# Kernel tuning notes

Measured on AMD Instinct MI355X. Metric: run time of the kernel, lower is better.

The kernel has to match this reference:

```python
import jax, jax.numpy as jnp
import numpy as np

HID = 64

def _rnn_layer(x, W_ih, W_hh, b_ih, b_hh):
    # x: [B, T, F]; PyTorch RNN step: h_t = tanh(x_t @ W_ih.T + b_ih + h_{t-1} @ W_hh.T + b_hh)
    # Precompute the input projection for all timesteps as one big GEMM.
    x_proj = jnp.einsum('btf,hf->bth', x, W_ih) + b_ih  # [B, T, H]
    B = x.shape[0]
    h0 = jnp.zeros((B, HID), x.dtype)

    def step(h, xt):
        h = jnp.tanh(xt + h @ W_hh.T + b_hh)
        return h, h

    _, hs = jax.lax.scan(step, h0, jnp.swapaxes(x_proj, 0, 1))  # hs: [T, B, H]
    return jnp.swapaxes(hs, 0, 1)  # [B, T, H]


def setup_inputs() -> dict:
    key = jax.random.key(0)
    ks = jax.random.split(key, 20)
    B, T, F = 4096, 128, 14
    s_in = 1.0 / np.sqrt(HID)  # PyTorch RNN init scale
    d = {
        'x': jax.random.normal(ks[0], (B, T, F), jnp.float32),
        'W_ih0': jax.random.normal(ks[1], (HID, F), jnp.float32) * s_in,
        'W_hh0': jax.random.normal(ks[2], (HID, HID), jnp.float32) * s_in,
        'b_ih0': jax.random.normal(ks[3], (HID,), jnp.float32) * s_in,
        'b_hh0': jax.random.normal(ks[4], (HID,), jnp.float32) * s_in,
        'W_ih1': jax.random.normal(ks[5], (HID, HID), jnp.float32) * s_in,
        'W_hh1': jax.random.normal(ks[6], (HID, HID), jnp.float32) * s_in,
        'b_ih1': jax.random.normal(ks[7], (HID,), jnp.float32) * s_in,
        'b_hh1': jax.random.normal(ks[8], (HID,), jnp.float32) * s_in,
        'W_ih2': jax.random.normal(ks[9], (HID, HID), jnp.float32) * s_in,
        'W_hh2': jax.random.normal(ks[10], (HID, HID), jnp.float32) * s_in,
        'b_ih2': jax.random.normal(ks[11], (HID,), jnp.float32) * s_in,
        'b_hh2': jax.random.normal(ks[12], (HID,), jnp.float32) * s_in,
        'fc1_w': jax.random.normal(ks[13], (32, HID), jnp.float32) * s_in,
        'fc1_b': jax.random.normal(ks[14], (32,), jnp.float32) * s_in,
        'fc2_w': jax.random.normal(ks[15], (1, 32), jnp.float32) * (1.0 / np.sqrt(32)),
        'fc2_b': jax.random.normal(ks[16], (1,), jnp.float32) * (1.0 / np.sqrt(32)),
    }
    return d


def reference(x, W_ih0, W_hh0, b_ih0, b_hh0, W_ih1, W_hh1, b_ih1, b_hh1,
              W_ih2, W_hh2, b_ih2, b_hh2, fc1_w, fc1_b, fc2_w, fc2_b):
    h = _rnn_layer(x, W_ih0, W_hh0, b_ih0, b_hh0)
    h = _rnn_layer(h, W_ih1, W_hh1, b_ih1, b_hh1)
    h = _rnn_layer(h, W_ih2, W_hh2, b_ih2, b_hh2)
    last = h[:, -1, :]                       # [B, H]
    y = jax.nn.relu(last @ fc1_w.T + fc1_b)  # [B, 32]
    return y @ fc2_w.T + fc2_b               # [B, 1]
```

## Files before the change

kernel.cpp:

```cpp
#include <hip/hip_runtime.h>

typedef short  s16x8 __attribute__((ext_vector_type(8)));
typedef float  f32x4 __attribute__((ext_vector_type(4)));
typedef float  f32x2 __attribute__((ext_vector_type(2)));
typedef unsigned int u32;
typedef unsigned int u32x4 __attribute__((ext_vector_type(4)));
typedef unsigned short u16;

#define DEVI static __device__ __forceinline__

#if __has_builtin(__builtin_amdgcn_exp2f)
#define EXP2(v) __builtin_amdgcn_exp2f(v)
#else
#define EXP2(v) exp2f(v)
#endif

constexpr int T_  = 128;
constexpr int F_  = 14;
constexpr int H_  = 64;
constexpr int BPB = 16;
constexpr int K_  = 8;
constexpr int NCH = T_ / K_;

constexpr int HF_BYTES   = 2 * 2 * K_ * 2 * 64 * 16;
constexpr int XBUF_BYTES = 2 * K_ * 64 * 16;
constexpr int SMEM_BYTES = HF_BYTES + XBUF_BYTES;

DEVI u16 f2bf(float f) {
  u32 u = __builtin_bit_cast(u32, f);
  u += 0x7fffu + ((u >> 16) & 1u);
  return (u16)(u >> 16);
}
DEVI u32 cvtpk(float a, float b) {
  u32 r;
  asm("v_cvt_pk_bf16_f32 %0, %1, %2" : "=v"(r) : "v"(a), "v"(b));
  return r;
}
DEVI s16x8 packfrag(const f32x4& a, const f32x4& b) {
  u32x4 p;
  p[0] = cvtpk(a[0], a[1]); p[1] = cvtpk(a[2], a[3]);
  p[2] = cvtpk(b[0], b[1]); p[3] = cvtpk(b[2], b[3]);
  return __builtin_bit_cast(s16x8, p);
}
DEVI f32x4 tanh4(const f32x4& v) {
  const f32x4 kC = -2.8853900817779268f;
  f32x4 t = v * kC;
  f32x4 e;
  e[0] = EXP2(t[0]); e[1] = EXP2(t[1]);
  e[2] = EXP2(t[2]); e[3] = EXP2(t[3]);
  const f32x4 kOne = 1.0f;
  f32x4 d = e + kOne;
  f32x4 r;
  r[0] = __builtin_amdgcn_rcpf(d[0]); r[1] = __builtin_amdgcn_rcpf(d[1]);
  r[2] = __builtin_amdgcn_rcpf(d[2]); r[3] = __builtin_amdgcn_rcpf(d[3]);
  const f32x4 kTwo = 2.0f, kNegOne = -1.0f;
  return __builtin_elementwise_fma(kTwo, r, kNegOne);
}
DEVI f32x4 MFMA(s16x8 a, s16x8 b, f32x4 c) {
  return __builtin_amdgcn_mfma_f32_16x16x32_bf16(a, b, c, 0, 0, 0);
}
DEVI s16x8 ldrow8(const float* p) {
  const f32x4 a = ((const f32x4*)p)[0];
  const f32x4 b = ((const f32x4*)p)[1];
  s16x8 r;
  r[0] = (short)f2bf(a[0]); r[1] = (short)f2bf(a[1]);
  r[2] = (short)f2bf(a[2]); r[3] = (short)f2bf(a[3]);
  r[4] = (short)f2bf(b[0]); r[5] = (short)f2bf(b[1]);
  r[6] = (short)f2bf(b[2]); r[7] = (short)f2bf(b[3]);
  return r;
}

__global__ __launch_bounds__(256, 1) void rnn_ck(
    const float* __restrict__ x,
    const float* __restrict__ Wih0, const float* __restrict__ Whh0,
    const float* __restrict__ bih0, const float* __restrict__ bhh0,
    const float* __restrict__ Wih1, const float* __restrict__ Whh1,
    const float* __restrict__ bih1, const float* __restrict__ bhh1,
    const float* __restrict__ Wih2, const float* __restrict__ Whh2,
    const float* __restrict__ bih2, const float* __restrict__ bhh2,
    const float* __restrict__ fc1w, const float* __restrict__ fc1b,
    const float* __restrict__ fc2w, const float* __restrict__ fc2b,
    float* __restrict__ out)
{
  extern __shared__ __align__(16) char smem[];
  u32x4 (*hf)[2][K_][2][64] = (u32x4 (*)[2][K_][2][64])smem;
  u32x4 (*xbuf)[K_][64]     = (u32x4 (*)[K_][64])(smem + HF_BYTES);

  const int tid  = threadIdx.x;
  const int w    = tid >> 6;
  const int lane = tid & 63;
  const int g    = lane >> 4;
  const int m    = lane & 15;
  const int b0   = blockIdx.x * BPB;

  f32x4 z4; z4[0] = 0.f; z4[1] = 0.f; z4[2] = 0.f; z4[3] = 0.f;

  s16x8 Ax[4], Ai[4][2], Ah[4][2];
  f32x4 bc[4];
  if (w < 3) {
    const float* Wi = Wih1; const float* Wh = Whh0;
    const float* bi = bih0; const float* bh = bhh0;
    if (w == 1)      { Wi = Wih1; Wh = Whh1; bi = bih1; bh = bhh1; }
    else if (w == 2) { Wi = Wih2; Wh = Whh2; bi = bih2; bh = bhh2; }
    #pragma unroll
    for (int n = 0; n < 4; n++) {
      const int Lr = 32 * (n & 1) + 8 * (m >> 2) + 4 * (n >> 1) + (m & 3);
      if (w == 0) {
        s16x8 r;
        #pragma unroll
        for (int j2 = 0; j2 < 8; j2++) {
          const int kk = 8 * g + j2;
          r[j2] = (kk < F_) ? (short)f2bf(Wih0[Lr * F_ + kk]) : (short)0;
        }
        Ax[n] = r;
        Ai[n][0] = r; Ai[n][1] = r;
      } else {
        #pragma unroll
        for (int kt = 0; kt < 2; kt++)
          Ai[n][kt] = ldrow8(Wi + Lr * H_ + 32 * kt + 8 * g);
        Ax[n] = Ai[n][0];
      }
      #pragma unroll
      for (int kt = 0; kt < 2; kt++)
        Ah[n][kt] = ldrow8(Wh + Lr * H_ + 32 * kt + 8 * g);
      const int Lb = 32 * (n & 1) + 8 * g + 4 * (n >> 1);
      bc[n] = *(const f32x4*)(bi + Lb) + *(const f32x4*)(bh + Lb);
    }
  }

  s16x8 F[2];
  {
    s16x8 z;
    #pragma unroll
    for (int i = 0; i < 8; i++) z[i] = 0;
    F[0] = z; F[1] = z;
  }
  f32x4 h2v[4];
  #pragma unroll
  for (int n = 0; n < 4; n++) h2v[n] = z4;

  const float* xrow = x + (size_t)(b0 + m) * T_ * F_;
  auto ldraw = [&](int t, f32x4& ra, f32x4& rb) {
    const float* p = xrow + t * F_;
    if (g == 0) {
      f32x2 p0 = *(const f32x2*)(p),     p1 = *(const f32x2*)(p + 2);
      f32x2 p2 = *(const f32x2*)(p + 4), p3 = *(const f32x2*)(p + 6);
      ra[0] = p0[0]; ra[1] = p0[1]; ra[2] = p1[0]; ra[3] = p1[1];
      rb[0] = p2[0]; rb[1] = p2[1]; rb[2] = p3[0]; rb[3] = p3[1];
    } else if (g == 1) {
      f32x2 p4 = *(const f32x2*)(p + 8), p5 = *(const f32x2*)(p + 10);
      f32x2 p6 = *(const f32x2*)(p + 12);
      ra[0] = p4[0]; ra[1] = p4[1]; ra[2] = p5[0]; ra[3] = p5[1];
      rb[0] = p6[0]; rb[1] = p6[1]; rb[2] = 0.f;   rb[3] = 0.f;
    } else {
      ra = z4; rb = z4;
    }
  };
  auto cvtraw = [&](const f32x4& ra, const f32x4& rb) -> s16x8 {
    u32x4 p;
    p[0] = cvtpk(ra[0], ra[1]); p[1] = cvtpk(ra[2], ra[3]);
    p[2] = cvtpk(rb[0], rb[1]); p[3] = cvtpk(rb[2], rb[3]);
    return __builtin_bit_cast(s16x8, p);
  };

  if (w == 3) {
    f32x4 ra[K_], rb[K_];
    #pragma unroll
    for (int k = 0; k < K_; k++) ldraw(k, ra[k], rb[k]);
    #pragma unroll
    for (int k = 0; k < K_; k++)
      xbuf[0][k][lane] = __builtin_bit_cast(u32x4, cvtraw(ra[k], rb[k]));
  }
  __syncthreads();

  #pragma unroll 1
  for (int e = 0; e < NCH + 2; e++) {
    const int wb = e & 1, rbuf = wb ^ 1;

    if (w == 3) {
      if (e < NCH - 1) {
        f32x4 ra[K_], rb[K_];
        #pragma unroll
        for (int k = 0; k < K_; k++) ldraw((e + 1) * K_ + k, ra[k], rb[k]);
        #pragma unroll
        for (int k = 0; k < K_; k++)
          xbuf[rbuf][k][lane] = __builtin_bit_cast(u32x4, cvtraw(ra[k], rb[k]));
      }
    } else {
      const int c = e - w;
      if (c >= 0 && c < NCH) {
        s16x8 cur[K_];
        f32x4 stage[2 * K_];
        if (w == 0) {
          #pragma unroll
          for (int k = 0; k < K_; k++)
            cur[k] = __builtin_bit_cast(s16x8, xbuf[wb][k][lane]);
        } else {
          const int src = w - 1;
          #pragma unroll
          for (int k = 0; k < K_; k++) {
            stage[k]      = __builtin_bit_cast(f32x4, hf[rbuf][src][k][0][lane]);
            stage[K_ + k] = __builtin_bit_cast(f32x4, hf[rbuf][src][k][1][lane]);
          }
        }

        f32x4 qc[4], qn[4];
        if (w == 0) {
          #pragma unroll
          for (int n = 0; n < 4; n++) qc[n] = MFMA(Ax[n], cur[0], bc[n]);
        } else {
          const s16x8 P0 = __builtin_bit_cast(s16x8, stage[0]);
          const s16x8 P1 = __builtin_bit_cast(s16x8, stage[K_]);
          #pragma unroll
          for (int n = 0; n < 4; n++) qc[n] = MFMA(Ai[n][0], P0, bc[n]);
          #pragma unroll
          for (int n = 0; n < 4; n++) qc[n] = MFMA(Ai[n][1], P1, qc[n]);
        }

        #pragma unroll
        for (int k = 0; k < K_; k++) {
          f32x4 p[4];
          p[0] = MFMA(Ah[0][0], F[0], qc[0]);
          p[2] = MFMA(Ah[2][0], F[0], qc[2]);
          p[1] = MFMA(Ah[1][0], F[0], qc[1]);
          p[3] = MFMA(Ah[3][0], F[0], qc[3]);
          p[0] = MFMA(Ah[0][1], F[1], p[0]);
          p[2] = MFMA(Ah[2][1], F[1], p[2]);
          p[1] = MFMA(Ah[1][1], F[1], p[1]);
          p[3] = MFMA(Ah[3][1], F[1], p[3]);

          if (k + 1 < K_) {
            if (w == 0) {
              #pragma unroll
              for (int n = 0; n < 4; n++) qn[n] = MFMA(Ax[n], cur[k + 1], bc[n]);
            } else {
              const s16x8 P0 = __builtin_bit_cast(s16x8, stage[k + 1]);
              const s16x8 P1 = __builtin_bit_cast(s16x8, stage[K_ + k + 1]);
              #pragma unroll
              for (int n = 0; n < 4; n++) qn[n] = MFMA(Ai[n][0], P0, bc[n]);
              #pragma unroll
              for (int n = 0; n < 4; n++) qn[n] = MFMA(Ai[n][1], P1, qn[n]);
            }
          }

          f32x4 hv0 = tanh4(p[0]);
          f32x4 hv2 = tanh4(p[2]);
          F[0] = packfrag(hv0, hv2);
          f32x4 hv1 = tanh4(p[1]);
          f32x4 hv3 = tanh4(p[3]);
          F[1] = packfrag(hv1, hv3);

          if (w < 2) {
            hf[wb][w][k][0][lane] = __builtin_bit_cast(u32x4, F[0]);
            hf[wb][w][k][1][lane] = __builtin_bit_cast(u32x4, F[1]);
          } else if (c == NCH - 1 && k == K_ - 1) {
            h2v[0] = hv0; h2v[1] = hv1;
            h2v[2] = hv2; h2v[3] = hv3;
          }

          if (k + 1 < K_) {
            #pragma unroll
            for (int n = 0; n < 4; n++) qc[n] = qn[n];
          }
        }
      }
    }
    __syncthreads();
  }

  float (*h2l)[68] = (float (*)[68])smem;
  if (w == 2) {
    #pragma unroll
    for (int n = 0; n < 4; n++) {
      const int Lb = 32 * (n & 1) + 8 * g + 4 * (n >> 1);
      *(f32x4*)&h2l[m][Lb] = h2v[n];
    }
  }
  __syncthreads();

  if (w == 0) {
    float hr[64];
    #pragma unroll
    for (int q = 0; q < 16; q++) {
      f32x4 v = *(const f32x4*)&h2l[m][4 * q];
      hr[4 * q + 0] = v[0]; hr[4 * q + 1] = v[1];
      hr[4 * q + 2] = v[2]; hr[4 * q + 3] = v[3];
    }
    float acc2 = 0.f;
    #pragma unroll
    for (int jj = 0; jj < 8; jj++) {
      const int jf = 8 * g + jj;
      float s = fc1b[jf];
      const f32x4* wp = (const f32x4*)(fc1w + jf * H_);
      #pragma unroll
      for (int kq = 0; kq < 16; kq++) {
        f32x4 wv = wp[kq];
        s += hr[4 * kq + 0] * wv[0] + hr[4 * kq + 1] * wv[1]
           + hr[4 * kq + 2] * wv[2] + hr[4 * kq + 3] * wv[3];
      }
      s = fmaxf(s, 0.f);
      acc2 += s * fc2w[jf];
    }
    acc2 += __shfl_xor(acc2, 16, 64);
    acc2 += __shfl_xor(acc2, 32, 64);
    if (lane < 16) out[b0 + m] = acc2 + fc2b[0];
  }
}

extern "C" void kernel_launch(void* const* d_in, const int* in_sizes, int n_in,
                              void* d_out, int out_size, void* d_ws, size_t ws_size,
                              hipStream_t stream) {
  const float* x    = (const float*)d_in[0];
  const float* Wih0 = (const float*)d_in[1];
  const float* Whh0 = (const float*)d_in[2];
  const float* bih0 = (const float*)d_in[3];
  const float* bhh0 = (const float*)d_in[4];
  const float* Wih1 = (const float*)d_in[5];
  const float* Whh1 = (const float*)d_in[6];
  const float* bih1 = (const float*)d_in[7];
  const float* bhh1 = (const float*)d_in[8];
  const float* Wih2 = (const float*)d_in[9];
  const float* Whh2 = (const float*)d_in[10];
  const float* bih2 = (const float*)d_in[11];
  const float* bhh2 = (const float*)d_in[12];
  const float* fc1w = (const float*)d_in[13];
  const float* fc1b = (const float*)d_in[14];
  const float* fc2w = (const float*)d_in[15];
  const float* fc2b = (const float*)d_in[16];

  static bool s_attr_set = false;
  if (!s_attr_set) {
    (void)hipFuncSetAttribute((const void*)rnn_ck,
                              hipFuncAttributeMaxDynamicSharedMemorySize,
                              SMEM_BYTES);
    s_attr_set = true;
  }

  rnn_ck<<<dim3(4096 / BPB), dim3(256), SMEM_BYTES, stream>>>(
      x, Wih0, Whh0, bih0, bhh0, Wih1, Whh1, bih1, bhh1,
      Wih2, Whh2, bih2, bhh2, fc1w, fc1b, fc2w, fc2b, (float*)d_out);
}
```

Measured before the change: 167.5 us.

## Split input projection and recurrence into separate wavefronts via LDS q-buffer

Doubles the block to 8 wavefronts. Three new A wavefronts compute the per-layer input projection (x or previous-layer h times W_ih plus biases) and write it to a new LDS qbuf. Three B wavefronts now run only the recurrent MFMA and tanh chain, reading the projection from qbuf. The chunk size shrinks from 8 to 4 and the pipeline deepens to 2 stages per layer. The aim is to take the input-projection MFMAs off the serial recurrence path. The cost is more LDS traffic, more block-wide barriers, a longer pipeline fill, and 7 active wavefronts (one idle) per block.

```diff
diff --git a/kernel.cpp b/kernel.cpp
--- a/kernel.cpp
+++ b/kernel.cpp
@@ -19,12 +19,13 @@
 constexpr int F_  = 14;
 constexpr int H_  = 64;
 constexpr int BPB = 16;
-constexpr int K_  = 8;
+constexpr int K_  = 4;
 constexpr int NCH = T_ / K_;
 
 constexpr int HF_BYTES   = 2 * 2 * K_ * 2 * 64 * 16;
 constexpr int XBUF_BYTES = 2 * K_ * 64 * 16;
-constexpr int SMEM_BYTES = HF_BYTES + XBUF_BYTES;
+constexpr int QBUF_BYTES = 2 * 3 * K_ * 4 * 64 * 16;
+constexpr int SMEM_BYTES = HF_BYTES + XBUF_BYTES + QBUF_BYTES;
 
 DEVI u16 f2bf(float f) {
   u32 u = __builtin_bit_cast(u32, f);
@@ -70,7 +71,7 @@
   return r;
 }
 
-__global__ __launch_bounds__(256, 1) void rnn_ck(
+__global__ __launch_bounds__(512, 1) void rnn_ck(
     const float* __restrict__ x,
     const float* __restrict__ Wih0, const float* __restrict__ Whh0,
     const float* __restrict__ bih0, const float* __restrict__ bhh0,
@@ -83,29 +84,45 @@
     float* __restrict__ out)
 {
   extern __shared__ __align__(16) char smem[];
-  u32x4 (*hf)[2][K_][2][64] = (u32x4 (*)[2][K_][2][64])smem;
-  u32x4 (*xbuf)[K_][64]     = (u32x4 (*)[K_][64])(smem + HF_BYTES);
+  u32x4 (*hf)[2][K_][2][64]   = (u32x4 (*)[2][K_][2][64])smem;
+  u32x4 (*xbuf)[K_][64]       = (u32x4 (*)[K_][64])(smem + HF_BYTES);
+  f32x4 (*qbuf)[3][K_][4][64] = (f32x4 (*)[3][K_][4][64])(smem + HF_BYTES + XBUF_BYTES);
 
   const int tid  = threadIdx.x;
-  const int w    = tid >> 6;
+  const int wv   = tid >> 6;
   const int lane = tid & 63;
   const int g    = lane >> 4;
   const int m    = lane & 15;
   const int b0   = blockIdx.x * BPB;
 
+  const bool isB = (wv < 3);
+  const bool isP = (wv == 3);
+  const bool isA = (wv >= 4 && wv < 7);
+  const int  l   = isB ? wv : (wv - 4);
+
   f32x4 z4; z4[0] = 0.f; z4[1] = 0.f; z4[2] = 0.f; z4[3] = 0.f;
+  s16x8 zf;
+  #pragma unroll
+  for (int i = 0; i < 8; i++) zf[i] = 0;
 
   s16x8 Ax[4], Ai[4][2], Ah[4][2];
   f32x4 bc[4];
-  if (w < 3) {
-    const float* Wi = Wih1; const float* Wh = Whh0;
-    const float* bi = bih0; const float* bh = bhh0;
-    if (w == 1)      { Wi = Wih1; Wh = Whh1; bi = bih1; bh = bhh1; }
-    else if (w == 2) { Wi = Wih2; Wh = Whh2; bi = bih2; bh = bhh2; }
+  if (isB) {
+    const float* Wh = (l == 0) ? Whh0 : (l == 1) ? Whh1 : Whh2;
     #pragma unroll
     for (int n = 0; n < 4; n++) {
       const int Lr = 32 * (n & 1) + 8 * (m >> 2) + 4 * (n >> 1) + (m & 3);
-      if (w == 0) {
+      Ah[n][0] = ldrow8(Wh + Lr * H_ + 8 * g);
+      Ah[n][1] = ldrow8(Wh + Lr * H_ + 32 + 8 * g);
+    }
+  } else if (isA) {
+    const float* Wi = (l == 1) ? Wih1 : Wih2;
+    const float* bi = (l == 0) ? bih0 : (l == 1) ? bih1 : bih2;
+    const float* bh = (l == 0) ? bhh0 : (l == 1) ? bhh1 : bhh2;
+    #pragma unroll
+    for (int n = 0; n < 4; n++) {
+      const int Lr = 32 * (n & 1) + 8 * (m >> 2) + 4 * (n >> 1) + (m & 3);
+      if (l == 0) {
         s16x8 r;
         #pragma unroll
         for (int j2 = 0; j2 < 8; j2++) {
@@ -113,28 +130,17 @@
           r[j2] = (kk < F_) ? (short)f2bf(Wih0[Lr * F_ + kk]) : (short)0;
         }
         Ax[n] = r;
-        Ai[n][0] = r; Ai[n][1] = r;
       } else {
-        #pragma unroll
-        for (int kt = 0; kt < 2; kt++)
-          Ai[n][kt] = ldrow8(Wi + Lr * H_ + 32 * kt + 8 * g);
-        Ax[n] = Ai[n][0];
+        Ai[n][0] = ldrow8(Wi + Lr * H_ + 8 * g);
+        Ai[n][1] = ldrow8(Wi + Lr * H_ + 32 + 8 * g);
       }
-      #pragma unroll
-      for (int kt = 0; kt < 2; kt++)
-        Ah[n][kt] = ldrow8(Wh + Lr * H_ + 32 * kt + 8 * g);
       const int Lb = 32 * (n & 1) + 8 * g + 4 * (n >> 1);
       bc[n] = *(const f32x4*)(bi + Lb) + *(const f32x4*)(bh + Lb);
     }
   }
 
   s16x8 F[2];
-  {
-    s16x8 z;
-    #pragma unroll
-    for (int i = 0; i < 8; i++) z[i] = 0;
-    F[0] = z; F[1] = z;
-  }
+  F[0] = zf; F[1] = zf;
   f32x4 h2v[4];
   #pragma unroll
   for (int n = 0; n < 4; n++) h2v[n] = z4;
@@ -162,86 +168,68 @@
     p[2] = cvtpk(rb[0], rb[1]); p[3] = cvtpk(rb[2], rb[3]);
     return __builtin_bit_cast(s16x8, p);
   };
-
-  if (w == 3) {
+  auto stage4 = [&](int par, int t0) {
     f32x4 ra[K_], rb[K_];
     #pragma unroll
-    for (int k = 0; k < K_; k++) ldraw(k, ra[k], rb[k]);
+    for (int k = 0; k < K_; k++) ldraw(t0 + k, ra[k], rb[k]);
     #pragma unroll
     for (int k = 0; k < K_; k++)
-      xbuf[0][k][lane] = __builtin_bit_cast(u32x4, cvtraw(ra[k], rb[k]));
-  }
+      xbuf[par][k][lane] = __builtin_bit_cast(u32x4, cvtraw(ra[k], rb[k]));
+  };
+
+  if (isP) stage4(0, 0);
   __syncthreads();
 
   #pragma unroll 1
-  for (int e = 0; e < NCH + 2; e++) {
+  for (int e = 0; e < NCH + 6; e++) {
     const int wb = e & 1, rbuf = wb ^ 1;
 
-    if (w == 3) {
-      if (e < NCH - 1) {
-        f32x4 ra[K_], rb[K_];
-        #pragma unroll
-        for (int k = 0; k < K_; k++) ldraw((e + 1) * K_ + k, ra[k], rb[k]);
-        #pragma unroll
-        for (int k = 0; k < K_; k++)
-          xbuf[rbuf][k][lane] = __builtin_bit_cast(u32x4, cvtraw(ra[k], rb[k]));
-      }
-    } else {
-      const int c = e - w;
+    if (isP) {
+      if (e >= 1 && e < NCH) stage4(wb, e * K_);
+    } else if (isA) {
+      const int c = e - (2 * l + 1);
       if (c >= 0 && c < NCH) {
-        s16x8 cur[K_];
-        f32x4 stage[2 * K_];
-        if (w == 0) {
-          #pragma unroll
-          for (int k = 0; k < K_; k++)
-            cur[k] = __builtin_bit_cast(s16x8, xbuf[wb][k][lane]);
-        } else {
-          const int src = w - 1;
+        if (l == 0) {
           #pragma unroll
           for (int k = 0; k < K_; k++) {
-            stage[k]      = __builtin_bit_cast(f32x4, hf[rbuf][src][k][0][lane]);
-            stage[K_ + k] = __builtin_bit_cast(f32x4, hf[rbuf][src][k][1][lane]);
+            const s16x8 xf = __builtin_bit_cast(s16x8, xbuf[rbuf][k][lane]);
+            #pragma unroll
+            for (int n = 0; n < 4; n++)
+              qbuf[wb][0][k][n][lane] = MFMA(Ax[n], xf, bc[n]);
+          }
+        } else {
+          #pragma unroll
+          for (int k = 0; k < K_; k++) {
+            const s16x8 P0 = __builtin_bit_cast(s16x8, hf[rbuf][l - 1][k][0][lane]);
+            const s16x8 P1 = __builtin_bit_cast(s16x8, hf[rbuf][l - 1][k][1][lane]);
+            f32x4 q[4];
+            #pragma unroll
+            for (int n = 0; n < 4; n++) q[n] = MFMA(Ai[n][0], P0, bc[n]);
+            #pragma unroll
+            for (int n = 0; n < 4; n++) q[n] = MFMA(Ai[n][1], P1, q[n]);
+            #pragma unroll
+            for (int n = 0; n < 4; n++) qbuf[wb][l][k][n][lane] = q[n];
           }
         }
-
-        f32x4 qc[4], qn[4];
-        if (w == 0) {
-          #pragma unroll
-          for (int n = 0; n < 4; n++) qc[n] = MFMA(Ax[n], cur[0], bc[n]);
-        } else {
-          const s16x8 P0 = __builtin_bit_cast(s16x8, stage[0]);
-          const s16x8 P1 = __builtin_bit_cast(s16x8, stage[K_]);
-          #pragma unroll
-          for (int n = 0; n < 4; n++) qc[n] = MFMA(Ai[n][0], P0, bc[n]);
-          #pragma unroll
-          for (int n = 0; n < 4; n++) qc[n] = MFMA(Ai[n][1], P1, qc[n]);
-        }
-
+      }
+    } else if (isB) {
+      const int c = e - (2 * l + 2);
+      if (c >= 0 && c < NCH) {
         #pragma unroll
         for (int k = 0; k < K_; k++) {
+          const f32x4 qc0 = qbuf[rbuf][l][k][0][lane];
+          const f32x4 qc1 = qbuf[rbuf][l][k][1][lane];
+          const f32x4 qc2 = qbuf[rbuf][l][k][2][lane];
+          const f32x4 qc3 = qbuf[rbuf][l][k][3][lane];
           f32x4 p[4];
-          p[0] = MFMA(Ah[0][0], F[0], qc[0]);
-          p[2] = MFMA(Ah[2][0], F[0], qc[2]);
-          p[1] = MFMA(Ah[1][0], F[0], qc[1]);
-          p[3] = MFMA(Ah[3][0], F[0], qc[3]);
+          p[0] = MFMA(Ah[0][0], F[0], qc0);
+          p[2] = MFMA(Ah[2][0], F[0], qc2);
+          p[1] = MFMA(Ah[1][0], F[0], qc1);
+          p[3] = MFMA(Ah[3][0], F[0], qc3);
           p[0] = MFMA(Ah[0][1], F[1], p[0]);
           p[2] = MFMA(Ah[2][1], F[1], p[2]);
           p[1] = MFMA(Ah[1][1], F[1], p[1]);
           p[3] = MFMA(Ah[3][1], F[1], p[3]);
-
-          if (k + 1 < K_) {
-            if (w == 0) {
-              #pragma unroll
-              for (int n = 0; n < 4; n++) qn[n] = MFMA(Ax[n], cur[k + 1], bc[n]);
-            } else {
-              const s16x8 P0 = __builtin_bit_cast(s16x8, stage[k + 1]);
-              const s16x8 P1 = __builtin_bit_cast(s16x8, stage[K_ + k + 1]);
-              #pragma unroll
-              for (int n = 0; n < 4; n++) qn[n] = MFMA(Ai[n][0], P0, bc[n]);
-              #pragma unroll
-              for (int n = 0; n < 4; n++) qn[n] = MFMA(Ai[n][1], P1, qn[n]);
-            }
-          }
 
           f32x4 hv0 = tanh4(p[0]);
           f32x4 hv2 = tanh4(p[2]);
@@ -250,18 +238,13 @@
           f32x4 hv3 = tanh4(p[3]);
           F[1] = packfrag(hv1, hv3);
 
-          if (w < 2) {
-            hf[wb][w][k][0][lane] = __builtin_bit_cast(u32x4, F[0]);
-            hf[wb][w][k][1][lane] = __builtin_bit_cast(u32x4, F[1]);
+          if (l < 2) {
+            hf[wb][l][k][0][lane] = __builtin_bit_cast(u32x4, F[0]);
+            hf[wb][l][k][1][lane] = __builtin_bit_cast(u32x4, F[1]);
           } else if (c == NCH - 1 && k == K_ - 1) {
             h2v[0] = hv0; h2v[1] = hv1;
             h2v[2] = hv2; h2v[3] = hv3;
           }
-
-          if (k + 1 < K_) {
-            #pragma unroll
-            for (int n = 0; n < 4; n++) qc[n] = qn[n];
-          }
         }
       }
     }
@@ -269,7 +252,7 @@
   }
 
   float (*h2l)[68] = (float (*)[68])smem;
-  if (w == 2) {
+  if (wv == 2) {
     #pragma unroll
     for (int n = 0; n < 4; n++) {
       const int Lb = 32 * (n & 1) + 8 * g + 4 * (n >> 1);
@@ -278,7 +261,7 @@
   }
   __syncthreads();
 
-  if (w == 0) {
+  if (wv == 0) {
     float hr[64];
     #pragma unroll
     for (int q = 0; q < 16; q++) {
@@ -294,9 +277,9 @@
       const f32x4* wp = (const f32x4*)(fc1w + jf * H_);
       #pragma unroll
       for (int kq = 0; kq < 16; kq++) {
-        f32x4 wv = wp[kq];
-        s += hr[4 * kq + 0] * wv[0] + hr[4 * kq + 1] * wv[1]
-           + hr[4 * kq + 2] * wv[2] + hr[4 * kq + 3] * wv[3];
+        f32x4 wv2 = wp[kq];
+        s += hr[4 * kq + 0] * wv2[0] + hr[4 * kq + 1] * wv2[1]
+           + hr[4 * kq + 2] * wv2[2] + hr[4 * kq + 3] * wv2[3];
       }
       s = fmaxf(s, 0.f);
       acc2 += s * fc2w[jf];
@@ -336,7 +319,7 @@
     s_attr_set = true;
   }
 
-  rnn_ck<<<dim3(4096 / BPB), dim3(256), SMEM_BYTES, stream>>>(
+  rnn_ck<<<dim3(4096 / BPB), dim3(512), SMEM_BYTES, stream>>>(
       x, Wih0, Whh0, bih0, bhh0, Wih1, Whh1, bih1, bhh1,
       Wih2, Whh2, bih2, bhh2, fc1w, fc1b, fc2w, fc2b, (float*)d_out);
 }
```

After: 160.7 us. 4.0% less time.
